# Optimization experiments

Measured on AMD Instinct MI355X. Metric: run time of the kernel, lower is better.

The kernel has to match this reference:

```python
import jax, jax.numpy as jnp
import numpy as np

LN_EPS = 1e-5

def setup_inputs() -> dict:
    key = jax.random.key(0)
    k1, k2, k3, k4 = jax.random.split(key, 4)
    B, N = 4, 4096
    inplanes, planes, loc_planes = 128, 128, 128
    img_fea = jax.random.normal(k1, (B, N, inplanes), dtype=jnp.float32)
    loc_fea = jax.random.normal(k2, (B, N, loc_planes), dtype=jnp.float32)
    # nn.Linear(loc_planes, inplanes*planes): weight (out, in), bias (out,)
    bound = 1.0 / np.sqrt(loc_planes)
    W = jax.random.uniform(k3, (inplanes * planes, loc_planes), minval=-bound, maxval=bound, dtype=jnp.float32)
    b = jax.random.uniform(k4, (inplanes * planes,), minval=-bound, maxval=bound, dtype=jnp.float32)
    gamma = jnp.ones((planes,), dtype=jnp.float32)
    beta = jnp.zeros((planes,), dtype=jnp.float32)
    return {"img_fea": img_fea, "loc_fea": loc_fea, "W": W, "b": b, "gamma": gamma, "beta": beta}

def reference(img_fea, loc_fea, W, b, gamma, beta):
    B, N, _ = loc_fea.shape
    inplanes = img_fea.shape[-1]
    # per-token weight generation: (B,N,loc) @ (loc, in*out) -> (B,N,in,out)
    w = (jnp.einsum('bnc,oc->bno', loc_fea, W) + b)
    planes = w.shape[-1] // inplanes
    w = w.reshape(B, N, inplanes, planes)
    # batched vec-matmul: (B,N,1,in) @ (B,N,in,out) -> (B,N,out)
    y = jnp.einsum('bni,bnio->bno', img_fea, w)
    # LayerNorm over last dim
    mu = jnp.mean(y, axis=-1, keepdims=True)
    var = jnp.mean(jnp.square(y - mu), axis=-1, keepdims=True)
    y = (y - mu) * jax.lax.rsqrt(var + LN_EPS) * gamma + beta
    return jax.nn.relu(y)
```

## Files before the change

kernel.cpp:

```cpp
#include <hip/hip_runtime.h>
#include <stdint.h>

using ushort8 = __attribute__((ext_vector_type(8))) unsigned short;
using bf16x8  = __attribute__((ext_vector_type(8))) __bf16;
using f32x16  = __attribute__((ext_vector_type(16))) float;

#define AS1 __attribute__((address_space(1)))
#define AS3 __attribute__((address_space(3)))

__device__ __forceinline__ unsigned short f2bf(float x){
  uint32_t u = __builtin_bit_cast(uint32_t, x);
  u = (u + 0x7FFFu + ((u >> 16) & 1u)) >> 16;
  return (unsigned short)u;
}
__device__ __forceinline__ float bf2f(unsigned short b){
  uint32_t u = ((uint32_t)b) << 16;
  return __builtin_bit_cast(float, u);
}

__device__ __forceinline__ f32x16 mfma16(bf16x8 a, bf16x8 b, f32x16 c){
  return __builtin_amdgcn_mfma_f32_32x32x16_bf16(a, b, c, 0, 0, 0);
}

__device__ __forceinline__ bf16x8 cvt8(const float* p){
  ushort8 v;
  #pragma unroll
  for (int j = 0; j < 8; ++j) v[j] = f2bf(p[j]);
  return __builtin_bit_cast(bf16x8, v);
}

__global__ void prep_wb2(const float* __restrict__ W, const float* __restrict__ bias,
                         unsigned short* __restrict__ Wb2){
  int e = blockIdx.x * 256 + threadIdx.x;
  if (e >= 129 * 16384) return;
  int jj = e & 7, w = (e >> 3) & 7, r = (e >> 6) & 31;
  int ch = (e >> 11) & 1, pt = (e >> 12) & 3, s = e >> 14;
  int p = pt * 32 + r, c = ch * 64 + w * 8 + jj;
  float v = (s < 128) ? W[(s << 14) + (p << 7) + c] : bias[(c << 7) + p];
  Wb2[e] = f2bf(v);
}

__global__ __launch_bounds__(512, 2)
void dynmlp(const float* __restrict__ img, const float* __restrict__ loc,
            const unsigned short* __restrict__ Wb2, float* __restrict__ part){
  __shared__ __align__(16) char smem[114688];
  unsigned short* imgT = (unsigned short*)(smem + 98304);
  float* ldsY = (float*)smem;

  const int tid = threadIdx.x, lane = tid & 63, wv = tid >> 6;
  const int pt = wv >> 1, ch = wv & 1;
  const int tt = blockIdx.x >> 1, h = blockIdx.x & 1;
  const int l31 = lane & 31, lg = lane >> 5;
  const int t0 = tt * 128;

  int goff[4];
  #pragma unroll
  for (int j = 0; j < 4; ++j){
    int slot = j * 64 + lane, r = slot >> 3, w = slot & 7;
    goff[j] = (r * 8 + (w ^ (r & 7))) * 16;
  }
  const char* slice0 = (const char*)Wb2 + (pt * 2 + ch) * 4096;
  char* ringb = smem + wv * 12288;

  auto STG = [&](int step, int buf){
    const char* g = slice0 + (size_t)step * 32768;
    char* l = ringb + buf * 4096 + (lane << 4);
    #pragma unroll
    for (int j = 0; j < 4; ++j)
      __builtin_amdgcn_global_load_lds((const AS1 uint32_t*)(g + goff[j]),
                                       (AS3 uint32_t*)(l + j * 1024), 16, 0, 0);
  };

  STG(h * 64 + 0, 0);
  STG(h * 64 + 1, 1);

  for (int e = tid; e < 2048; e += 512){
    int tl = e >> 4, iq = e & 15;
    float4 v = *(const float4*)&img[(size_t)(t0 + tl) * 128 + h * 64 + iq * 4];
    int a = iq * 4 * 128 + tl;
    imgT[a]       = f2bf(v.x);
    imgT[a + 128] = f2bf(v.y);
    imgT[a + 256] = f2bf(v.z);
    imgT[a + 384] = f2bf(v.w);
  }

  bf16x8 bfr[4][4];
  #pragma unroll
  for (int f = 0; f < 4; ++f){
    int t = t0 + f * 32 + l31;
    #pragma unroll
    for (int cc = 0; cc < 4; ++cc)
      bfr[f][cc] = cvt8(&loc[(size_t)t * 128 + ch * 64 + cc * 16 + lg * 8]);
  }

  int aoff[4];
  #pragma unroll
  for (int cc = 0; cc < 4; ++cc)
    aoff[cc] = (l31 * 8 + ((cc * 2 + lg) ^ (l31 & 7))) * 16;

  __syncthreads();

  f32x16 acc[4] = {{}, {}, {}, {}};
  const unsigned short* imgRow = imgT + l31;

  auto computeStep = [&](int buf, int ki){
    const char* bufp = ringb + buf * 4096;
    f32x16 S0 = {}, S1 = {}, S2 = {}, S3 = {};
    __builtin_amdgcn_s_setprio(1);
    #pragma unroll
    for (int cc = 0; cc < 4; ++cc){
      bf16x8 a = *(const bf16x8*)(bufp + aoff[cc]);
      S0 = mfma16(a, bfr[0][cc], S0);
      S1 = mfma16(a, bfr[1][cc], S1);
      S2 = mfma16(a, bfr[2][cc], S2);
      S3 = mfma16(a, bfr[3][cc], S3);
    }
    __builtin_amdgcn_s_setprio(0);
    float s0 = bf2f(imgRow[ki * 128]);
    float s1 = bf2f(imgRow[ki * 128 + 32]);
    float s2 = bf2f(imgRow[ki * 128 + 64]);
    float s3 = bf2f(imgRow[ki * 128 + 96]);
    acc[0] += S0 * s0; acc[1] += S1 * s1; acc[2] += S2 * s2; acc[3] += S3 * s3;
  };

  int bcur = 0;
  for (int ki = 0; ki < 62; ++ki){
    int bpre = bcur + 2; if (bpre >= 3) bpre -= 3;
    STG(h * 64 + ki + 2, bpre);
    asm volatile("s_waitcnt vmcnt(8)" ::: "memory");
    computeStep(bcur, ki);
    bcur = (bcur == 2) ? 0 : bcur + 1;
  }
  if (h == 0){
    STG(128, 1);
    asm volatile("s_waitcnt vmcnt(8)" ::: "memory");
  } else {
    asm volatile("s_waitcnt vmcnt(4)" ::: "memory");
  }
  computeStep(2, 62);
  if (h == 0){
    asm volatile("s_waitcnt vmcnt(4)" ::: "memory");
  } else {
    asm volatile("s_waitcnt vmcnt(0)" ::: "memory");
  }
  computeStep(0, 63);
  if (h == 0){
    asm volatile("s_waitcnt vmcnt(0)" ::: "memory");
    const char* bufp = ringb + 1 * 4096;
    #pragma unroll
    for (int cc = 0; cc < 4; ++cc){
      bf16x8 a = *(const bf16x8*)(bufp + aoff[cc]);
      #pragma unroll
      for (int f = 0; f < 4; ++f){
        bf16x8 bi = cvt8(&img[(size_t)(t0 + f * 32 + l31) * 128 + ch * 64 + cc * 16 + lg * 8]);
        acc[f] = mfma16(a, bi, acc[f]);
      }
    }
  }

  __syncthreads();
  if (ch == 0){
    #pragma unroll
    for (int f = 0; f < 4; ++f){
      int t_l = f * 32 + l31;
      #pragma unroll
      for (int r = 0; r < 16; ++r){
        int p = pt * 32 + (r & 3) + 8 * (r >> 2) + 4 * lg;
        ldsY[t_l * 129 + p] = acc[f][r];
      }
    }
  }
  __syncthreads();
  if (ch == 1){
    #pragma unroll
    for (int f = 0; f < 4; ++f){
      int t_l = f * 32 + l31;
      #pragma unroll
      for (int r = 0; r < 16; ++r){
        int p = pt * 32 + (r & 3) + 8 * (r >> 2) + 4 * lg;
        ldsY[t_l * 129 + p] += acc[f][r];
      }
    }
  }
  __syncthreads();
  float* dst = part + ((size_t)h * 16384 + t0) * 128;
  #pragma unroll
  for (int k = 0; k < 8; ++k){
    int idx4 = k * 512 + tid;
    int t_l = idx4 >> 5, q = idx4 & 31;
    const float* s = &ldsY[t_l * 129 + q * 4];
    float4 v = {s[0], s[1], s[2], s[3]};
    *(float4*)&dst[t_l * 128 + q * 4] = v;
  }
}

__global__ __launch_bounds__(512)
void lnk(const float* __restrict__ part, const float* __restrict__ gamma,
         const float* __restrict__ beta, float* __restrict__ out){
  const int tid = threadIdx.x, lane = tid & 63, wv = tid >> 6;
  const float* p0 = part;
  const float* p1 = part + (size_t)16384 * 128;
  float g0  = gamma[lane], g1 = gamma[lane + 64];
  float be0 = beta[lane],  be1 = beta[lane + 64];
  int tb = blockIdx.x * 64 + wv * 8;
  #pragma unroll 1
  for (int k = 0; k < 8; ++k){
    size_t t = tb + k;
    float y0 = p0[t * 128 + lane]      + p1[t * 128 + lane];
    float y1 = p0[t * 128 + 64 + lane] + p1[t * 128 + 64 + lane];
    float s = y0 + y1, sq = y0 * y0 + y1 * y1;
    #pragma unroll
    for (int m = 32; m >= 1; m >>= 1){
      s  += __shfl_xor(s, m, 64);
      sq += __shfl_xor(sq, m, 64);
    }
    float mean = s * (1.0f / 128.0f);
    float var  = sq * (1.0f / 128.0f) - mean * mean;
    float rs   = rsqrtf(var + 1e-5f);
    float o0 = fmaxf((y0 - mean) * rs * g0 + be0, 0.0f);
    float o1 = fmaxf((y1 - mean) * rs * g1 + be1, 0.0f);
    out[t * 128 + lane]      = o0;
    out[t * 128 + 64 + lane] = o1;
  }
}

extern "C" void kernel_launch(void* const* d_in, const int* in_sizes, int n_in,
                              void* d_out, int out_size, void* d_ws, size_t ws_size,
                              hipStream_t stream){
  const float* img   = (const float*)d_in[0];
  const float* loc   = (const float*)d_in[1];
  const float* W     = (const float*)d_in[2];
  const float* bias  = (const float*)d_in[3];
  const float* gamma = (const float*)d_in[4];
  const float* beta  = (const float*)d_in[5];
  float* out = (float*)d_out;
  unsigned short* Wb2 = (unsigned short*)d_ws;
  float* part = (float*)((char*)d_ws + 4227072);

  prep_wb2<<<8256, 256, 0, stream>>>(W, bias, Wb2);
  dynmlp<<<256, 512, 0, stream>>>(img, loc, Wb2, part);
  lnk<<<256, 512, 0, stream>>>(part, gamma, beta, out);
}
```

Before: 95.70 us.

## Deepen weight ring to four stages, stagger block phases, pre-swizzle weights

```diff
diff --git a/kernel.cpp b/kernel.cpp
--- a/kernel.cpp
+++ b/kernel.cpp
@@ -35,7 +35,8 @@
   if (e >= 129 * 16384) return;
   int jj = e & 7, w = (e >> 3) & 7, r = (e >> 6) & 31;
   int ch = (e >> 11) & 1, pt = (e >> 12) & 3, s = e >> 14;
-  int p = pt * 32 + r, c = ch * 64 + w * 8 + jj;
+  int p = pt * 32 + r;
+  int c = ch * 64 + ((w ^ (r & 7)) << 3) + jj;
   float v = (s < 128) ? W[(s << 14) + (p << 7) + c] : bias[(c << 7) + p];
   Wb2[e] = f2bf(v);
 }
@@ -43,36 +44,45 @@
 __global__ __launch_bounds__(512, 2)
 void dynmlp(const float* __restrict__ img, const float* __restrict__ loc,
             const unsigned short* __restrict__ Wb2, float* __restrict__ part){
-  __shared__ __align__(16) char smem[114688];
-  unsigned short* imgT = (unsigned short*)(smem + 98304);
+  __shared__ __align__(16) char smem[147456];
+  unsigned short* imgT = (unsigned short*)(smem + 131072);
   float* ldsY = (float*)smem;
 
+  const int b = blockIdx.x;
+  const int h     = (b >> 2) & 1;
+  const int tt    = ((b >> 3) << 2) | (b & 3);
+  const int phase = b >> 3;
   const int tid = threadIdx.x, lane = tid & 63, wv = tid >> 6;
   const int pt = wv >> 1, ch = wv & 1;
-  const int tt = blockIdx.x >> 1, h = blockIdx.x & 1;
   const int l31 = lane & 31, lg = lane >> 5;
   const int t0 = tt * 128;
 
-  int goff[4];
-  #pragma unroll
-  for (int j = 0; j < 4; ++j){
-    int slot = j * 64 + lane, r = slot >> 3, w = slot & 7;
-    goff[j] = (r * 8 + (w ^ (r & 7))) * 16;
-  }
-  const char* slice0 = (const char*)Wb2 + (pt * 2 + ch) * 4096;
-  char* ringb = smem + wv * 12288;
-
-  auto STG = [&](int step, int buf){
-    const char* g = slice0 + (size_t)step * 32768;
-    char* l = ringb + buf * 4096 + (lane << 4);
+  char* ringb = smem + wv * 16384;
+  const char* sliceBase = (const char*)Wb2 +
+      ((size_t)(h * 64) * 8 + (size_t)(pt * 2 + ch)) * 4096 + (lane << 4);
+  const char* biasSrc = (const char*)Wb2 +
+      ((size_t)128 * 8 + (size_t)(pt * 2 + ch)) * 4096 + (lane << 4);
+
+  auto stg = [&](int psLocal, char* ldst){
+    const char* g = sliceBase + (size_t)psLocal * 32768;
+    char* l = ldst + (lane << 4);
     #pragma unroll
     for (int j = 0; j < 4; ++j)
-      __builtin_amdgcn_global_load_lds((const AS1 uint32_t*)(g + goff[j]),
+      __builtin_amdgcn_global_load_lds((const AS1 uint32_t*)(g + j * 1024),
                                        (AS3 uint32_t*)(l + j * 1024), 16, 0, 0);
   };
-
-  STG(h * 64 + 0, 0);
-  STG(h * 64 + 1, 1);
+  auto stgB = [&](char* ldst){
+    char* l = ldst + (lane << 4);
+    #pragma unroll
+    for (int j = 0; j < 4; ++j)
+      __builtin_amdgcn_global_load_lds((const AS1 uint32_t*)(biasSrc + j * 1024),
+                                       (AS3 uint32_t*)(l + j * 1024), 16, 0, 0);
+  };
+  #define LP(k) (((k) + phase) & 63)
+
+  stg(LP(0), ringb);
+  stg(LP(1), ringb + 4096);
+  stg(LP(2), ringb + 8192);
 
   for (int e = tid; e < 2048; e += 512){
     int tl = e >> 4, iq = e & 15;
@@ -101,10 +111,10 @@
   __syncthreads();
 
   f32x16 acc[4] = {{}, {}, {}, {}};
-  const unsigned short* imgRow = imgT + l31;
-
-  auto computeStep = [&](int buf, int ki){
-    const char* bufp = ringb + buf * 4096;
+
+  auto cstep = [&](const char* bufp, int ps){
+    const unsigned short* ir = imgT + ps * 128 + l31;
+    float s0 = bf2f(ir[0]), s1 = bf2f(ir[32]), s2 = bf2f(ir[64]), s3 = bf2f(ir[96]);
     f32x16 S0 = {}, S1 = {}, S2 = {}, S3 = {};
     __builtin_amdgcn_s_setprio(1);
     #pragma unroll
@@ -116,37 +126,36 @@
       S3 = mfma16(a, bfr[3][cc], S3);
     }
     __builtin_amdgcn_s_setprio(0);
-    float s0 = bf2f(imgRow[ki * 128]);
-    float s1 = bf2f(imgRow[ki * 128 + 32]);
-    float s2 = bf2f(imgRow[ki * 128 + 64]);
-    float s3 = bf2f(imgRow[ki * 128 + 96]);
     acc[0] += S0 * s0; acc[1] += S1 * s1; acc[2] += S2 * s2; acc[3] += S3 * s3;
   };
 
-  int bcur = 0;
-  for (int ki = 0; ki < 62; ++ki){
-    int bpre = bcur + 2; if (bpre >= 3) bpre -= 3;
-    STG(h * 64 + ki + 2, bpre);
+  for (int kb = 0; kb < 60; kb += 4){
+    #define BODY(J, PB) \
+      stg(LP(kb + (J) + 3), ringb + (PB) * 4096); \
+      asm volatile("s_waitcnt vmcnt(12)" ::: "memory"); \
+      cstep(ringb + (J) * 4096, LP(kb + (J)));
+    BODY(0, 3) BODY(1, 0) BODY(2, 1) BODY(3, 2)
+    #undef BODY
+  }
+  stg(LP(63), ringb + 3 * 4096);
+  asm volatile("s_waitcnt vmcnt(12)" ::: "memory");
+  cstep(ringb, LP(60));
+  if (h == 0){
+    stgB(ringb);
+    asm volatile("s_waitcnt vmcnt(12)" ::: "memory");
+  } else {
     asm volatile("s_waitcnt vmcnt(8)" ::: "memory");
-    computeStep(bcur, ki);
-    bcur = (bcur == 2) ? 0 : bcur + 1;
-  }
-  if (h == 0){
-    STG(128, 1);
-    asm volatile("s_waitcnt vmcnt(8)" ::: "memory");
-  } else {
-    asm volatile("s_waitcnt vmcnt(4)" ::: "memory");
-  }
-  computeStep(2, 62);
-  if (h == 0){
-    asm volatile("s_waitcnt vmcnt(4)" ::: "memory");
-  } else {
-    asm volatile("s_waitcnt vmcnt(0)" ::: "memory");
-  }
-  computeStep(0, 63);
+  }
+  cstep(ringb + 4096, LP(61));
+  if (h == 0) asm volatile("s_waitcnt vmcnt(8)" ::: "memory");
+  else        asm volatile("s_waitcnt vmcnt(4)" ::: "memory");
+  cstep(ringb + 8192, LP(62));
+  if (h == 0) asm volatile("s_waitcnt vmcnt(4)" ::: "memory");
+  else        asm volatile("s_waitcnt vmcnt(0)" ::: "memory");
+  cstep(ringb + 12288, LP(63));
   if (h == 0){
     asm volatile("s_waitcnt vmcnt(0)" ::: "memory");
-    const char* bufp = ringb + 1 * 4096;
+    const char* bufp = ringb;
     #pragma unroll
     for (int cc = 0; cc < 4; ++cc){
       bf16x8 a = *(const bf16x8*)(bufp + aoff[cc]);
```

Result: slower. 109.4 us (+14.3%).

## Load weight slices directly into registers with double-buffering instead of LDS ring

Applied to the files above, without the earlier changes.

```diff
diff --git a/kernel.cpp b/kernel.cpp
--- a/kernel.cpp
+++ b/kernel.cpp
@@ -4,9 +4,9 @@
 using ushort8 = __attribute__((ext_vector_type(8))) unsigned short;
 using bf16x8  = __attribute__((ext_vector_type(8))) __bf16;
 using f32x16  = __attribute__((ext_vector_type(16))) float;
-
-#define AS1 __attribute__((address_space(1)))
-#define AS3 __attribute__((address_space(3)))
+using f32x2   = __attribute__((ext_vector_type(2))) float;
+using u32x4   = __attribute__((ext_vector_type(4))) uint32_t;
+using us4     = __attribute__((ext_vector_type(4))) unsigned short;
 
 __device__ __forceinline__ unsigned short f2bf(float x){
   uint32_t u = __builtin_bit_cast(uint32_t, x);
@@ -29,59 +29,45 @@
   return __builtin_bit_cast(bf16x8, v);
 }
 
-__global__ void prep_wb2(const float* __restrict__ W, const float* __restrict__ bias,
-                         unsigned short* __restrict__ Wb2){
+__global__ void prep_wb3(const float* __restrict__ W, const float* __restrict__ bias,
+                         unsigned short* __restrict__ Wb3){
   int e = blockIdx.x * 256 + threadIdx.x;
   if (e >= 129 * 16384) return;
   int jj = e & 7, w = (e >> 3) & 7, r = (e >> 6) & 31;
   int ch = (e >> 11) & 1, pt = (e >> 12) & 3, s = e >> 14;
-  int p = pt * 32 + r, c = ch * 64 + w * 8 + jj;
+  int p = pt * 32 + r;
+  int c = ch * 64 + w * 8 + jj;
   float v = (s < 128) ? W[(s << 14) + (p << 7) + c] : bias[(c << 7) + p];
-  Wb2[e] = f2bf(v);
+  Wb3[e] = f2bf(v);
 }
 
 __global__ __launch_bounds__(512, 2)
 void dynmlp(const float* __restrict__ img, const float* __restrict__ loc,
-            const unsigned short* __restrict__ Wb2, float* __restrict__ part){
-  __shared__ __align__(16) char smem[114688];
-  unsigned short* imgT = (unsigned short*)(smem + 98304);
+            const unsigned short* __restrict__ Wb3, float* __restrict__ part){
+  __shared__ __align__(16) char smem[66048];
+  unsigned short* imgT = (unsigned short*)smem;
   float* ldsY = (float*)smem;
 
+  const int b = blockIdx.x;
+  const int tt = b >> 1, h = b & 1;
   const int tid = threadIdx.x, lane = tid & 63, wv = tid >> 6;
   const int pt = wv >> 1, ch = wv & 1;
-  const int tt = blockIdx.x >> 1, h = blockIdx.x & 1;
   const int l31 = lane & 31, lg = lane >> 5;
   const int t0 = tt * 128;
 
-  int goff[4];
-  #pragma unroll
-  for (int j = 0; j < 4; ++j){
-    int slot = j * 64 + lane, r = slot >> 3, w = slot & 7;
-    goff[j] = (r * 8 + (w ^ (r & 7))) * 16;
-  }
-  const char* slice0 = (const char*)Wb2 + (pt * 2 + ch) * 4096;
-  char* ringb = smem + wv * 12288;
-
-  auto STG = [&](int step, int buf){
-    const char* g = slice0 + (size_t)step * 32768;
-    char* l = ringb + buf * 4096 + (lane << 4);
-    #pragma unroll
-    for (int j = 0; j < 4; ++j)
-      __builtin_amdgcn_global_load_lds((const AS1 uint32_t*)(g + goff[j]),
-                                       (AS3 uint32_t*)(l + j * 1024), 16, 0, 0);
-  };
-
-  STG(h * 64 + 0, 0);
-  STG(h * 64 + 1, 1);
+  const char* wslice = (const char*)Wb3 +
+      ((size_t)(h * 64) * 8 + (size_t)(pt * 2 + ch)) * 4096 + l31 * 128;
+  const char* biasSl = (const char*)Wb3 +
+      ((size_t)128 * 8 + (size_t)(pt * 2 + ch)) * 4096 + l31 * 128;
 
   for (int e = tid; e < 2048; e += 512){
-    int tl = e >> 4, iq = e & 15;
+    int tl = e & 127, iq = e >> 7;
     float4 v = *(const float4*)&img[(size_t)(t0 + tl) * 128 + h * 64 + iq * 4];
-    int a = iq * 4 * 128 + tl;
-    imgT[a]       = f2bf(v.x);
-    imgT[a + 128] = f2bf(v.y);
-    imgT[a + 256] = f2bf(v.z);
-    imgT[a + 384] = f2bf(v.w);
+    int slot = (tl & 31) * 4 + (tl >> 5);
+    imgT[(iq * 4 + 0) * 128 + slot] = f2bf(v.x);
+    imgT[(iq * 4 + 1) * 128 + slot] = f2bf(v.y);
+    imgT[(iq * 4 + 2) * 128 + slot] = f2bf(v.z);
+    imgT[(iq * 4 + 3) * 128 + slot] = f2bf(v.w);
   }
 
   bf16x8 bfr[4][4];
@@ -93,67 +79,101 @@
       bfr[f][cc] = cvt8(&loc[(size_t)t * 128 + ch * 64 + cc * 16 + lg * 8]);
   }
 
-  int aoff[4];
-  #pragma unroll
-  for (int cc = 0; cc < 4; ++cc)
-    aoff[cc] = (l31 * 8 + ((cc * 2 + lg) ^ (l31 & 7))) * 16;
-
-  __syncthreads();
-
-  f32x16 acc[4] = {{}, {}, {}, {}};
-  const unsigned short* imgRow = imgT + l31;
-
-  auto computeStep = [&](int buf, int ki){
-    const char* bufp = ringb + buf * 4096;
-    f32x16 S0 = {}, S1 = {}, S2 = {}, S3 = {};
-    __builtin_amdgcn_s_setprio(1);
-    #pragma unroll
-    for (int cc = 0; cc < 4; ++cc){
-      bf16x8 a = *(const bf16x8*)(bufp + aoff[cc]);
-      S0 = mfma16(a, bfr[0][cc], S0);
-      S1 = mfma16(a, bfr[1][cc], S1);
-      S2 = mfma16(a, bfr[2][cc], S2);
-      S3 = mfma16(a, bfr[3][cc], S3);
-    }
-    __builtin_amdgcn_s_setprio(0);
-    float s0 = bf2f(imgRow[ki * 128]);
-    float s1 = bf2f(imgRow[ki * 128 + 32]);
-    float s2 = bf2f(imgRow[ki * 128 + 64]);
-    float s3 = bf2f(imgRow[ki * 128 + 96]);
-    acc[0] += S0 * s0; acc[1] += S1 * s1; acc[2] += S2 * s2; acc[3] += S3 * s3;
-  };
-
-  int bcur = 0;
-  for (int ki = 0; ki < 62; ++ki){
-    int bpre = bcur + 2; if (bpre >= 3) bpre -= 3;
-    STG(h * 64 + ki + 2, bpre);
-    asm volatile("s_waitcnt vmcnt(8)" ::: "memory");
-    computeStep(bcur, ki);
-    bcur = (bcur == 2) ? 0 : bcur + 1;
-  }
+  f32x16 Z;
+  #pragma unroll
+  for (int i = 0; i < 16; ++i) Z[i] = 0.0f;
+  asm volatile("" : "+v"(Z));
+
+  f32x2 accp[4][8];
+  #pragma unroll
+  for (int f = 0; f < 4; ++f)
+    #pragma unroll
+    for (int q = 0; q < 8; ++q) accp[f][q] = (f32x2){0.0f, 0.0f};
+
+  u32x4 avA[4], avB[4];
+  {
+    const u32x4* g = (const u32x4*)wslice;
+    #pragma unroll
+    for (int i = 0; i < 4; ++i) avA[i] = g[i * 2 + lg];
+  }
+  const char* gp = wslice + 32768;
+
+  __syncthreads();
+
+  const unsigned short* imgP = imgT + l31 * 4;
+
+  #define STEPBODY(AV, W4) do { \
+    bf16x8 a0 = __builtin_bit_cast(bf16x8, AV[0]); \
+    bf16x8 a1 = __builtin_bit_cast(bf16x8, AV[1]); \
+    bf16x8 a2 = __builtin_bit_cast(bf16x8, AV[2]); \
+    bf16x8 a3 = __builtin_bit_cast(bf16x8, AV[3]); \
+    __builtin_amdgcn_s_setprio(1); \
+    f32x16 T0 = mfma16(a0, bfr[0][0], Z); \
+    f32x16 T1 = mfma16(a0, bfr[1][0], Z); \
+    f32x16 T2 = mfma16(a0, bfr[2][0], Z); \
+    f32x16 T3 = mfma16(a0, bfr[3][0], Z); \
+    T0 = mfma16(a1, bfr[0][1], T0); T1 = mfma16(a1, bfr[1][1], T1); \
+    T2 = mfma16(a1, bfr[2][1], T2); T3 = mfma16(a1, bfr[3][1], T3); \
+    T0 = mfma16(a2, bfr[0][2], T0); T1 = mfma16(a2, bfr[1][2], T1); \
+    T2 = mfma16(a2, bfr[2][2], T2); T3 = mfma16(a2, bfr[3][2], T3); \
+    T0 = mfma16(a3, bfr[0][3], T0); T1 = mfma16(a3, bfr[1][3], T1); \
+    T2 = mfma16(a3, bfr[2][3], T2); T3 = mfma16(a3, bfr[3][3], T3); \
+    __builtin_amdgcn_s_setprio(0); \
+    float s0 = bf2f(W4[0]), s1 = bf2f(W4[1]), s2 = bf2f(W4[2]), s3 = bf2f(W4[3]); \
+    f32x2 v0 = {s0, s0}, v1 = {s1, s1}, v2 = {s2, s2}, v3 = {s3, s3}; \
+    _Pragma("unroll") \
+    for (int q = 0; q < 8; ++q){ \
+      f32x2 p0 = {T0[2*q], T0[2*q+1]}; \
+      f32x2 p1 = {T1[2*q], T1[2*q+1]}; \
+      f32x2 p2 = {T2[2*q], T2[2*q+1]}; \
+      f32x2 p3 = {T3[2*q], T3[2*q+1]}; \
+      asm("v_pk_fma_f32 %0, %1, %2, %0" : "+v"(accp[0][q]) : "v"(p0), "v"(v0)); \
+      asm("v_pk_fma_f32 %0, %1, %2, %0" : "+v"(accp[1][q]) : "v"(p1), "v"(v1)); \
+      asm("v_pk_fma_f32 %0, %1, %2, %0" : "+v"(accp[2][q]) : "v"(p2), "v"(v2)); \
+      asm("v_pk_fma_f32 %0, %1, %2, %0" : "+v"(accp[3][q]) : "v"(p3), "v"(v3)); \
+    } \
+  } while (0)
+
+  for (int k = 0; k < 64; k += 2){
+    us4 w0 = *(const us4*)(imgP + k * 128);
+    {
+      const u32x4* g = (const u32x4*)gp;
+      #pragma unroll
+      for (int i = 0; i < 4; ++i) avB[i] = g[i * 2 + lg];
+      gp += 32768;
+    }
+    STEPBODY(avA, w0);
+
+    us4 w1 = *(const us4*)(imgP + (k + 1) * 128);
+    if (k + 2 < 64){
+      const u32x4* g = (const u32x4*)gp;
+      #pragma unroll
+      for (int i = 0; i < 4; ++i) avA[i] = g[i * 2 + lg];
+      gp += 32768;
+    } else if (h == 0){
+      const u32x4* g = (const u32x4*)biasSl;
+      #pragma unroll
+      for (int i = 0; i < 4; ++i) avA[i] = g[i * 2 + lg];
+    }
+    STEPBODY(avB, w1);
+  }
+
   if (h == 0){
-    STG(128, 1);
-    asm volatile("s_waitcnt vmcnt(8)" ::: "memory");
-  } else {
-    asm volatile("s_waitcnt vmcnt(4)" ::: "memory");
-  }
-  computeStep(2, 62);
-  if (h == 0){
-    asm volatile("s_waitcnt vmcnt(4)" ::: "memory");
-  } else {
-    asm volatile("s_waitcnt vmcnt(0)" ::: "memory");
-  }
-  computeStep(0, 63);
-  if (h == 0){
-    asm volatile("s_waitcnt vmcnt(0)" ::: "memory");
-    const char* bufp = ringb + 1 * 4096;
-    #pragma unroll
-    for (int cc = 0; cc < 4; ++cc){
-      bf16x8 a = *(const bf16x8*)(bufp + aoff[cc]);
-      #pragma unroll
-      for (int f = 0; f < 4; ++f){
-        bf16x8 bi = cvt8(&img[(size_t)(t0 + f * 32 + l31) * 128 + ch * 64 + cc * 16 + lg * 8]);
-        acc[f] = mfma16(a, bi, acc[f]);
+    bf16x8 a0 = __builtin_bit_cast(bf16x8, avA[0]);
+    bf16x8 a1 = __builtin_bit_cast(bf16x8, avA[1]);
+    bf16x8 a2 = __builtin_bit_cast(bf16x8, avA[2]);
+    bf16x8 a3 = __builtin_bit_cast(bf16x8, avA[3]);
+    #pragma unroll
+    for (int f = 0; f < 4; ++f){
+      size_t tr = (size_t)(t0 + f * 32 + l31) * 128 + ch * 64 + lg * 8;
+      f32x16 T = mfma16(a0, cvt8(&img[tr]),      Z);
+      T = mfma16(a1, cvt8(&img[tr + 16]), T);
+      T = mfma16(a2, cvt8(&img[tr + 32]), T);
+      T = mfma16(a3, cvt8(&img[tr + 48]), T);
+      #pragma unroll
+      for (int q = 0; q < 8; ++q){
+        accp[f][q][0] += T[2*q];
+        accp[f][q][1] += T[2*q+1];
       }
     }
   }
@@ -166,7 +186,7 @@
       #pragma unroll
       for (int r = 0; r < 16; ++r){
         int p = pt * 32 + (r & 3) + 8 * (r >> 2) + 4 * lg;
-        ldsY[t_l * 129 + p] = acc[f][r];
+        ldsY[t_l * 129 + p] = accp[f][r >> 1][r & 1];
       }
     }
   }
@@ -178,7 +198,7 @@
       #pragma unroll
       for (int r = 0; r < 16; ++r){
         int p = pt * 32 + (r & 3) + 8 * (r >> 2) + 4 * lg;
-        ldsY[t_l * 129 + p] += acc[f][r];
+        ldsY[t_l * 129 + p] += accp[f][r >> 1][r & 1];
       }
     }
   }
@@ -234,10 +254,10 @@
   const float* gamma = (const float*)d_in[4];
   const float* beta  = (const float*)d_in[5];
   float* out = (float*)d_out;
-  unsigned short* Wb2 = (unsigned short*)d_ws;
+  unsigned short* Wb3 = (unsigned short*)d_ws;
   float* part = (float*)((char*)d_ws + 4227072);
 
-  prep_wb2<<<8256, 256, 0, stream>>>(W, bias, Wb2);
-  dynmlp<<<256, 512, 0, stream>>>(img, loc, Wb2, part);
+  prep_wb3<<<8256, 256, 0, stream>>>(W, bias, Wb3);
+  dynmlp<<<256, 512, 0, stream>>>(img, loc, Wb3, part);
   lnk<<<256, 512, 0, stream>>>(part, gamma, beta, out);
 }
```

Result: slower. 109.3 us (+14.2%).
